# Optimization experiments

Measured on AMD Instinct MI355X. Metric: run time of the kernel, lower is better.

The kernel has to match this reference:

```python
import jax, jax.numpy as jnp
import numpy as np

B, N = 64, 4096

def setup_inputs() -> dict:
    key = jax.random.key(0)
    k1, k2, k3, k4, k5, k6 = jax.random.split(key, 6)
    return {
        "V_mag": jax.random.uniform(k1, (B, N), dtype=jnp.float32, minval=0.9, maxval=1.1),
        "V_ang": 0.3 * jax.random.normal(k2, (B, N), dtype=jnp.float32),
        "P_in": jax.random.normal(k3, (B, N), dtype=jnp.float32),
        "Q_in": jax.random.normal(k4, (B, N), dtype=jnp.float32),
        "G_bus": jax.random.normal(k5, (N, N), dtype=jnp.float32) / np.sqrt(N),
        "B_bus": jax.random.normal(k6, (N, N), dtype=jnp.float32) / np.sqrt(N),
    }

def reference(V_mag, V_ang, P_in, Q_in, G_bus, B_bus):
    # P_i = V_i sum_j V_j (G_ij cos(ti-tj) + B_ij sin(ti-tj))
    # Q_i = V_i sum_j V_j (G_ij sin(ti-tj) - B_ij cos(ti-tj))
    # Angle-addition rewrite (exact): with c_j = V_j cos(t_j), s_j = V_j sin(t_j):
    #   sum_j G_ij V_j cos(ti-tj) = cos(ti)*(G c)_i + sin(ti)*(G s)_i, etc.
    cos_t = jnp.cos(V_ang)  # [B, N]
    sin_t = jnp.sin(V_ang)
    c = V_mag * cos_t       # V_j cos(t_j)
    s = V_mag * sin_t       # V_j sin(t_j)
    Gc = jnp.einsum('ij,bj->bi', G_bus, c)
    Gs = jnp.einsum('ij,bj->bi', G_bus, s)
    Bc = jnp.einsum('ij,bj->bi', B_bus, c)
    Bs = jnp.einsum('ij,bj->bi', B_bus, s)
    # sum_j V_j (G cos + B sin) = cos_ti*(Gc+Bs) + sin_ti*(Gs-Bc)
    P_calc = V_mag * (cos_t * (Gc + Bs) + sin_t * (Gs - Bc))
    # sum_j V_j (G sin - B cos) = sin_ti*(Gc+Bs) - cos_ti*(Gs-Bc)
    Q_calc = V_mag * (sin_t * (Gc + Bs) - cos_t * (Gs - Bc))
    res_P = P_calc - P_in
    res_Q = Q_calc - Q_in
    return (res_P, res_Q)
```

## Files before the change

kernel.cpp:

```cpp
#include <hip/hip_runtime.h>
#include <stdint.h>

#define N_DIM 4096
#define B_DIM 64

typedef __bf16 bf16x8 __attribute__((ext_vector_type(8)));
typedef float floatx4 __attribute__((ext_vector_type(4)));

union FragU { uint4 u; bf16x8 h; };

__device__ __forceinline__ unsigned short f2bf_rne(float f) {
    unsigned int u = __float_as_uint(f);
    u += 0x7fffu + ((u >> 16) & 1u);
    return (unsigned short)(u >> 16);
}

__global__ __launch_bounds__(256) void pf_prep(
        const float* __restrict__ Vmag, const float* __restrict__ Vang,
        unsigned short* __restrict__ c_pk, unsigned short* __restrict__ s_pk,
        float* __restrict__ c_f, float* __restrict__ s_f) {
    int idx = blockIdx.x * 256 + threadIdx.x;
    int b = idx >> 12;
    int j = idx & 4095;
    float sv, cv;
    sincosf(Vang[idx], &sv, &cv);
    float v = Vmag[idx];
    float c = v * cv;
    float s = v * sv;
    c_f[idx] = c;
    s_f[idx] = s;
    int p = (((j >> 3) << 6) + b) * 8 + (j & 7);
    c_pk[p] = f2bf_rne(c);
    s_pk[p] = f2bf_rne(s);
}

__global__ __launch_bounds__(1024, 4) void pf_gemm(
        const float* __restrict__ G, const float* __restrict__ Bm,
        const unsigned short* __restrict__ c_pk, const unsigned short* __restrict__ s_pk,
        const float* __restrict__ c_f, const float* __restrict__ s_f,
        const float* __restrict__ P_in, const float* __restrict__ Q_in,
        float* __restrict__ out) {
    __shared__ float red[2][8][16][66];
    const int tid = threadIdx.x;
    const int wave = tid >> 6;
    const int lane = tid & 63;
    const int n = lane & 15;
    const int quad = lane >> 4;
    const int i0 = blockIdx.x << 4;
    const int kw = wave << 8;

    const float* gp = G  + (size_t)(i0 + n) * N_DIM + kw + (quad << 3);
    const float* bp = Bm + (size_t)(i0 + n) * N_DIM + kw + (quad << 3);
    const unsigned short* cp = c_pk + ((size_t)(((kw >> 3) + quad) << 6) + n) * 8;
    const unsigned short* sp = s_pk + ((size_t)(((kw >> 3) + quad) << 6) + n) * 8;

    floatx4 accX[4], accY[4];
    #pragma unroll
    for (int t = 0; t < 4; ++t) {
        accX[t] = (floatx4){0.f, 0.f, 0.f, 0.f};
        accY[t] = (floatx4){0.f, 0.f, 0.f, 0.f};
    }

    float4 g0 = *(const float4*)gp;
    float4 g1 = *(const float4*)(gp + 4);
    float4 h0 = *(const float4*)bp;
    float4 h1 = *(const float4*)(bp + 4);
    gp += 32; bp += 32;

    #pragma unroll 1
    for (int it = 0; it < 8; ++it) {
        float4 ng0, ng1, nh0, nh1;
        if (it < 7) {
            ng0 = *(const float4*)gp;
            ng1 = *(const float4*)(gp + 4);
            nh0 = *(const float4*)bp;
            nh1 = *(const float4*)(bp + 4);
            gp += 32; bp += 32;
        }

        uint4 cu[4];
        #pragma unroll
        for (int t = 0; t < 4; ++t) cu[t] = *(const uint4*)(cp + t * 128);
        cp += 2048;

        bf16x8 ag, ah;
        ag[0] = (__bf16)g0.x; ag[1] = (__bf16)g0.y; ag[2] = (__bf16)g0.z; ag[3] = (__bf16)g0.w;
        ag[4] = (__bf16)g1.x; ag[5] = (__bf16)g1.y; ag[6] = (__bf16)g1.z; ag[7] = (__bf16)g1.w;
        ah[0] = (__bf16)h0.x; ah[1] = (__bf16)h0.y; ah[2] = (__bf16)h0.z; ah[3] = (__bf16)h0.w;
        ah[4] = (__bf16)h1.x; ah[5] = (__bf16)h1.y; ah[6] = (__bf16)h1.z; ah[7] = (__bf16)h1.w;

        #pragma unroll
        for (int t = 0; t < 4; ++t) {
            FragU cf, nf;
            cf.u = cu[t];
            nf.u.x = cu[t].x ^ 0x80008000u;
            nf.u.y = cu[t].y ^ 0x80008000u;
            nf.u.z = cu[t].z ^ 0x80008000u;
            nf.u.w = cu[t].w ^ 0x80008000u;
            accX[t] = __builtin_amdgcn_mfma_f32_16x16x32_bf16(ag, cf.h, accX[t], 0, 0, 0);
            accY[t] = __builtin_amdgcn_mfma_f32_16x16x32_bf16(ah, nf.h, accY[t], 0, 0, 0);
        }

        uint4 su[4];
        #pragma unroll
        for (int t = 0; t < 4; ++t) su[t] = *(const uint4*)(sp + t * 128);
        sp += 2048;

        #pragma unroll
        for (int t = 0; t < 4; ++t) {
            FragU sf;
            sf.u = su[t];
            accX[t] = __builtin_amdgcn_mfma_f32_16x16x32_bf16(ah, sf.h, accX[t], 0, 0, 0);
            accY[t] = __builtin_amdgcn_mfma_f32_16x16x32_bf16(ag, sf.h, accY[t], 0, 0, 0);
        }

        if (it < 7) { g0 = ng0; g1 = ng1; h0 = nh0; h1 = nh1; }
    }

    if (wave >= 8) {
        #pragma unroll
        for (int t = 0; t < 4; ++t) {
            #pragma unroll
            for (int r = 0; r < 4; ++r) {
                red[0][wave - 8][(quad << 2) + r][(t << 4) + n] = accX[t][r];
                red[1][wave - 8][(quad << 2) + r][(t << 4) + n] = accY[t][r];
            }
        }
    }
    __syncthreads();
    if (wave < 8) {
        #pragma unroll
        for (int t = 0; t < 4; ++t) {
            #pragma unroll
            for (int r = 0; r < 4; ++r) {
                red[0][wave][(quad << 2) + r][(t << 4) + n] += accX[t][r];
                red[1][wave][(quad << 2) + r][(t << 4) + n] += accY[t][r];
            }
        }
    }
    __syncthreads();

    {
        int bb = tid >> 4;
        int m = tid & 15;
        float X = 0.f, Y = 0.f;
        #pragma unroll
        for (int w = 0; w < 8; ++w) {
            X += red[0][w][m][bb];
            Y += red[1][w][m][bb];
        }
        size_t off = (size_t)bb * N_DIM + i0 + m;
        float c = c_f[off], s = s_f[off];
        out[off] = c * X + s * Y - P_in[off];
        out[(size_t)B_DIM * N_DIM + off] = s * X - c * Y - Q_in[off];
    }
}

extern "C" void kernel_launch(void* const* d_in, const int* in_sizes, int n_in,
                              void* d_out, int out_size, void* d_ws, size_t ws_size,
                              hipStream_t stream) {
    const float* Vmag = (const float*)d_in[0];
    const float* Vang = (const float*)d_in[1];
    const float* P_in = (const float*)d_in[2];
    const float* Q_in = (const float*)d_in[3];
    const float* G    = (const float*)d_in[4];
    const float* Bm   = (const float*)d_in[5];
    float* out = (float*)d_out;

    char* ws = (char*)d_ws;
    unsigned short* c_pk = (unsigned short*)(ws);
    unsigned short* s_pk = (unsigned short*)(ws + (512u << 10));
    float* c_f = (float*)(ws + (1u << 20));
    float* s_f = (float*)(ws + (2u << 20));

    hipLaunchKernelGGL(pf_prep, dim3((B_DIM * N_DIM) / 256), dim3(256), 0, stream,
                       Vmag, Vang, c_pk, s_pk, c_f, s_f);
    hipLaunchKernelGGL(pf_gemm, dim3(N_DIM / 16), dim3(1024), 0, stream,
                       G, Bm, c_pk, s_pk, c_f, s_f, P_in, Q_in, out);
}
```

Measured before the change: 171.9 us.

## Stage G/B tiles through LDS via direct global-to-LDS loads with double buffering

The G and B row tiles are now loaded into shared memory with direct global-to-LDS transfers, where each wave fetches a full contiguous row segment, and the loads are double-buffered across eight K chunks. Before, each wave read its own strided K-slice into registers. Waves now read their MFMA A-fragments from LDS, and the K split is interleaved per chunk instead of giving each wave a contiguous 256-column block. The goal is more coalesced HBM traffic and fewer VGPRs spent on prefetch. In exchange it adds a block-wide barrier per chunk and about 132 KB of LDS per block, which likely limits each CU to one resident block.

```diff
diff --git a/kernel.cpp b/kernel.cpp
--- a/kernel.cpp
+++ b/kernel.cpp
@@ -8,6 +8,14 @@
 typedef float floatx4 __attribute__((ext_vector_type(4)));
 
 union FragU { uint4 u; bf16x8 h; };
+
+#define AS1 __attribute__((address_space(1)))
+#define AS3 __attribute__((address_space(3)))
+
+__device__ __forceinline__ void gll16(const float* gp, float* lp) {
+    __builtin_amdgcn_global_load_lds((const AS1 void*)(const void*)gp,
+                                     (AS3 void*)(void*)lp, 16, 0, 0);
+}
 
 __device__ __forceinline__ unsigned short f2bf_rne(float f) {
     unsigned int u = __float_as_uint(f);
@@ -34,25 +42,31 @@
     s_pk[p] = f2bf_rne(s);
 }
 
+#define ROWF 516
+#define MATF (16 * ROWF)
+#define BUFF (2 * MATF)
 __global__ __launch_bounds__(1024, 4) void pf_gemm(
         const float* __restrict__ G, const float* __restrict__ Bm,
         const unsigned short* __restrict__ c_pk, const unsigned short* __restrict__ s_pk,
         const float* __restrict__ c_f, const float* __restrict__ s_f,
         const float* __restrict__ P_in, const float* __restrict__ Q_in,
         float* __restrict__ out) {
-    __shared__ float red[2][8][16][66];
+    __shared__ __align__(16) float lds_f[2 * BUFF];
     const int tid = threadIdx.x;
     const int wave = tid >> 6;
     const int lane = tid & 63;
     const int n = lane & 15;
     const int quad = lane >> 4;
     const int i0 = blockIdx.x << 4;
-    const int kw = wave << 8;
 
-    const float* gp = G  + (size_t)(i0 + n) * N_DIM + kw + (quad << 3);
-    const float* bp = Bm + (size_t)(i0 + n) * N_DIM + kw + (quad << 3);
-    const unsigned short* cp = c_pk + ((size_t)(((kw >> 3) + quad) << 6) + n) * 8;
-    const unsigned short* sp = s_pk + ((size_t)(((kw >> 3) + quad) << 6) + n) * 8;
+    const float* gsrc = G  + (size_t)(i0 + wave) * N_DIM + lane * 4;
+    const float* bsrc = Bm + (size_t)(i0 + wave) * N_DIM + lane * 4;
+    const int stg = wave * ROWF;
+
+    const int aoff = n * ROWF + wave * 32 + quad * 8;
+
+    const unsigned short* cp = c_pk + ((size_t)(((wave << 2) + quad) << 6) + n) * 8;
+    const unsigned short* sp = s_pk + ((size_t)(((wave << 2) + quad) << 6) + n) * 8;
 
     floatx4 accX[4], accY[4];
     #pragma unroll
@@ -61,34 +75,41 @@
         accY[t] = (floatx4){0.f, 0.f, 0.f, 0.f};
     }
 
-    float4 g0 = *(const float4*)gp;
-    float4 g1 = *(const float4*)(gp + 4);
-    float4 h0 = *(const float4*)bp;
-    float4 h1 = *(const float4*)(bp + 4);
-    gp += 32; bp += 32;
+    gll16(gsrc,       lds_f + stg);
+    gll16(gsrc + 256, lds_f + stg + 256);
+    gll16(bsrc,       lds_f + MATF + stg);
+    gll16(bsrc + 256, lds_f + MATF + stg + 256);
 
-    #pragma unroll 1
-    for (int it = 0; it < 8; ++it) {
-        float4 ng0, ng1, nh0, nh1;
-        if (it < 7) {
-            ng0 = *(const float4*)gp;
-            ng1 = *(const float4*)(gp + 4);
-            nh0 = *(const float4*)bp;
-            nh1 = *(const float4*)(bp + 4);
-            gp += 32; bp += 32;
+    #pragma unroll 2
+    for (int c = 0; c < 8; ++c) {
+        const int buf = (c & 1) * BUFF;
+        __syncthreads();
+
+        if (c < 7) {
+            const int nb = ((c + 1) & 1) * BUFF;
+            const float* gs = gsrc + (c + 1) * 512;
+            const float* bs = bsrc + (c + 1) * 512;
+            gll16(gs,       lds_f + nb + stg);
+            gll16(gs + 256, lds_f + nb + stg + 256);
+            gll16(bs,       lds_f + nb + MATF + stg);
+            gll16(bs + 256, lds_f + nb + MATF + stg + 256);
         }
 
-        uint4 cu[4];
-        #pragma unroll
-        for (int t = 0; t < 4; ++t) cu[t] = *(const uint4*)(cp + t * 128);
-        cp += 2048;
-
+        const float* ga = lds_f + buf + aoff;
+        const float* ba = lds_f + buf + MATF + aoff;
+        float4 g0 = *(const float4*)ga;
+        float4 g1 = *(const float4*)(ga + 4);
+        float4 h0 = *(const float4*)ba;
+        float4 h1 = *(const float4*)(ba + 4);
         bf16x8 ag, ah;
         ag[0] = (__bf16)g0.x; ag[1] = (__bf16)g0.y; ag[2] = (__bf16)g0.z; ag[3] = (__bf16)g0.w;
         ag[4] = (__bf16)g1.x; ag[5] = (__bf16)g1.y; ag[6] = (__bf16)g1.z; ag[7] = (__bf16)g1.w;
         ah[0] = (__bf16)h0.x; ah[1] = (__bf16)h0.y; ah[2] = (__bf16)h0.z; ah[3] = (__bf16)h0.w;
         ah[4] = (__bf16)h1.x; ah[5] = (__bf16)h1.y; ah[6] = (__bf16)h1.z; ah[7] = (__bf16)h1.w;
 
+        uint4 cu[4];
+        #pragma unroll
+        for (int t = 0; t < 4; ++t) cu[t] = *(const uint4*)(cp + (size_t)c * 32768 + t * 128);
         #pragma unroll
         for (int t = 0; t < 4; ++t) {
             FragU cf, nf;
@@ -103,9 +124,7 @@
 
         uint4 su[4];
         #pragma unroll
-        for (int t = 0; t < 4; ++t) su[t] = *(const uint4*)(sp + t * 128);
-        sp += 2048;
-
+        for (int t = 0; t < 4; ++t) su[t] = *(const uint4*)(sp + (size_t)c * 32768 + t * 128);
         #pragma unroll
         for (int t = 0; t < 4; ++t) {
             FragU sf;
@@ -113,30 +132,29 @@
             accX[t] = __builtin_amdgcn_mfma_f32_16x16x32_bf16(ah, sf.h, accX[t], 0, 0, 0);
             accY[t] = __builtin_amdgcn_mfma_f32_16x16x32_bf16(ag, sf.h, accY[t], 0, 0, 0);
         }
-
-        if (it < 7) { g0 = ng0; g1 = ng1; h0 = nh0; h1 = nh1; }
     }
 
+    float* red = lds_f;
+    #define RED(x, wp, m, b) red[(((x) * 8 + (wp)) * 16 + (m)) * 66 + (b)]
+    __syncthreads();
     if (wave >= 8) {
         #pragma unroll
-        for (int t = 0; t < 4; ++t) {
+        for (int t = 0; t < 4; ++t)
             #pragma unroll
             for (int r = 0; r < 4; ++r) {
-                red[0][wave - 8][(quad << 2) + r][(t << 4) + n] = accX[t][r];
-                red[1][wave - 8][(quad << 2) + r][(t << 4) + n] = accY[t][r];
+                RED(0, wave - 8, (quad << 2) + r, (t << 4) + n) = accX[t][r];
+                RED(1, wave - 8, (quad << 2) + r, (t << 4) + n) = accY[t][r];
             }
-        }
     }
     __syncthreads();
     if (wave < 8) {
         #pragma unroll
-        for (int t = 0; t < 4; ++t) {
+        for (int t = 0; t < 4; ++t)
             #pragma unroll
             for (int r = 0; r < 4; ++r) {
-                red[0][wave][(quad << 2) + r][(t << 4) + n] += accX[t][r];
-                red[1][wave][(quad << 2) + r][(t << 4) + n] += accY[t][r];
+                RED(0, wave, (quad << 2) + r, (t << 4) + n) += accX[t][r];
+                RED(1, wave, (quad << 2) + r, (t << 4) + n) += accY[t][r];
             }
-        }
     }
     __syncthreads();
 
@@ -146,8 +164,8 @@
         float X = 0.f, Y = 0.f;
         #pragma unroll
         for (int w = 0; w < 8; ++w) {
-            X += red[0][w][m][bb];
-            Y += red[1][w][m][bb];
+            X += RED(0, w, m, bb);
+            Y += RED(1, w, m, bb);
         }
         size_t off = (size_t)bb * N_DIM + i0 + m;
         float c = c_f[off], s = s_f[off];
```

Result: faster. 163.7 us (-4.7%).

## Split GEMM over K across blocks with workspace partials and separate reduce kernel

Applied to the files above, without the earlier changes.

Each block now covers 64 output rows and a quarter of K. Its 16 waves form 4 row stripes by 4 K sub-chunks, so the c/s fragment loads are shared across stripes within the block. Partial X/Y sums go to a workspace and a new pf_reduce kernel sums the four K chunks and applies the cos/sin epilogue. The c/s loads are also hoisted to the top of each loop iteration. The cost is an extra kernel launch plus about 8 MB of workspace traffic.

```diff
diff --git a/kernel.cpp b/kernel.cpp
--- a/kernel.cpp
+++ b/kernel.cpp
@@ -3,6 +3,7 @@
 
 #define N_DIM 4096
 #define B_DIM 64
+#define OUTSZ (B_DIM * N_DIM)
 
 typedef __bf16 bf16x8 __attribute__((ext_vector_type(8)));
 typedef float floatx4 __attribute__((ext_vector_type(4)));
@@ -37,22 +38,26 @@
 __global__ __launch_bounds__(1024, 4) void pf_gemm(
         const float* __restrict__ G, const float* __restrict__ Bm,
         const unsigned short* __restrict__ c_pk, const unsigned short* __restrict__ s_pk,
-        const float* __restrict__ c_f, const float* __restrict__ s_f,
-        const float* __restrict__ P_in, const float* __restrict__ Q_in,
-        float* __restrict__ out) {
-    __shared__ float red[2][8][16][66];
+        float* __restrict__ ws_part) {
+    __shared__ float redX[3][4][16][66];
+    __shared__ float redY[3][4][16][66];
     const int tid = threadIdx.x;
     const int wave = tid >> 6;
     const int lane = tid & 63;
     const int n = lane & 15;
     const int quad = lane >> 4;
-    const int i0 = blockIdx.x << 4;
-    const int kw = wave << 8;
-
-    const float* gp = G  + (size_t)(i0 + n) * N_DIM + kw + (quad << 3);
-    const float* bp = Bm + (size_t)(i0 + n) * N_DIM + kw + (quad << 3);
-    const unsigned short* cp = c_pk + ((size_t)(((kw >> 3) + quad) << 6) + n) * 8;
-    const unsigned short* sp = s_pk + ((size_t)(((kw >> 3) + quad) << 6) + n) * 8;
+    const int kc = blockIdx.x & 3;
+    const int rg = blockIdx.x >> 2;
+    const int stripe = wave & 3;
+    const int kq = wave >> 2;
+
+    const int row = (rg << 6) + (stripe << 4) + n;
+    const int kb = (kc << 10) + (kq << 8);
+
+    const float* gp = G  + (size_t)row * N_DIM + kb + (quad << 3);
+    const float* bp = Bm + (size_t)row * N_DIM + kb + (quad << 3);
+    const unsigned short* cp = c_pk + ((size_t)((kb >> 3) + quad) * 64 + n) * 8;
+    const unsigned short* sp = s_pk + ((size_t)((kb >> 3) + quad) * 64 + n) * 8;
 
     floatx4 accX[4], accY[4];
     #pragma unroll
@@ -69,6 +74,13 @@
 
     #pragma unroll 1
     for (int it = 0; it < 8; ++it) {
+        uint4 cu[4], su[4];
+        #pragma unroll
+        for (int t = 0; t < 4; ++t) cu[t] = *(const uint4*)(cp + t * 128);
+        #pragma unroll
+        for (int t = 0; t < 4; ++t) su[t] = *(const uint4*)(sp + t * 128);
+        cp += 2048; sp += 2048;
+
         float4 ng0, ng1, nh0, nh1;
         if (it < 7) {
             ng0 = *(const float4*)gp;
@@ -77,11 +89,6 @@
             nh1 = *(const float4*)(bp + 4);
             gp += 32; bp += 32;
         }
-
-        uint4 cu[4];
-        #pragma unroll
-        for (int t = 0; t < 4; ++t) cu[t] = *(const uint4*)(cp + t * 128);
-        cp += 2048;
 
         bf16x8 ag, ah;
         ag[0] = (__bf16)g0.x; ag[1] = (__bf16)g0.y; ag[2] = (__bf16)g0.z; ag[3] = (__bf16)g0.w;
@@ -100,12 +107,6 @@
             accX[t] = __builtin_amdgcn_mfma_f32_16x16x32_bf16(ag, cf.h, accX[t], 0, 0, 0);
             accY[t] = __builtin_amdgcn_mfma_f32_16x16x32_bf16(ah, nf.h, accY[t], 0, 0, 0);
         }
-
-        uint4 su[4];
-        #pragma unroll
-        for (int t = 0; t < 4; ++t) su[t] = *(const uint4*)(sp + t * 128);
-        sp += 2048;
-
         #pragma unroll
         for (int t = 0; t < 4; ++t) {
             FragU sf;
@@ -117,43 +118,67 @@
         if (it < 7) { g0 = ng0; g1 = ng1; h0 = nh0; h1 = nh1; }
     }
 
-    if (wave >= 8) {
-        #pragma unroll
-        for (int t = 0; t < 4; ++t) {
+    if (kq > 0) {
+        #pragma unroll
+        for (int t = 0; t < 4; ++t)
             #pragma unroll
             for (int r = 0; r < 4; ++r) {
-                red[0][wave - 8][(quad << 2) + r][(t << 4) + n] = accX[t][r];
-                red[1][wave - 8][(quad << 2) + r][(t << 4) + n] = accY[t][r];
+                redX[kq - 1][stripe][(quad << 2) + r][(t << 4) + n] = accX[t][r];
+                redY[kq - 1][stripe][(quad << 2) + r][(t << 4) + n] = accY[t][r];
             }
-        }
     }
     __syncthreads();
-    if (wave < 8) {
-        #pragma unroll
-        for (int t = 0; t < 4; ++t) {
+    if (kq == 0) {
+        #pragma unroll
+        for (int t = 0; t < 4; ++t)
             #pragma unroll
             for (int r = 0; r < 4; ++r) {
-                red[0][wave][(quad << 2) + r][(t << 4) + n] += accX[t][r];
-                red[1][wave][(quad << 2) + r][(t << 4) + n] += accY[t][r];
+                float x = accX[t][r], y = accY[t][r];
+                #pragma unroll
+                for (int w = 0; w < 3; ++w) {
+                    x += redX[w][stripe][(quad << 2) + r][(t << 4) + n];
+                    y += redY[w][stripe][(quad << 2) + r][(t << 4) + n];
+                }
+                accX[t][r] = x; accY[t][r] = y;
             }
-        }
-    }
-    __syncthreads();
-
-    {
-        int bb = tid >> 4;
-        int m = tid & 15;
-        float X = 0.f, Y = 0.f;
-        #pragma unroll
-        for (int w = 0; w < 8; ++w) {
-            X += red[0][w][m][bb];
-            Y += red[1][w][m][bb];
-        }
-        size_t off = (size_t)bb * N_DIM + i0 + m;
-        float c = c_f[off], s = s_f[off];
-        out[off] = c * X + s * Y - P_in[off];
-        out[(size_t)B_DIM * N_DIM + off] = s * X - c * Y - Q_in[off];
-    }
+        float* wsX = ws_part + (size_t)kc * OUTSZ;
+        float* wsY = ws_part + (size_t)(4 + kc) * OUTSZ;
+        const int rowbase = (rg << 6) + (stripe << 4) + (quad << 2);
+        #pragma unroll
+        for (int t = 0; t < 4; ++t) {
+            size_t off = (size_t)((t << 4) + n) * N_DIM + rowbase;
+            *(float4*)(wsX + off) = (float4){accX[t][0], accX[t][1], accX[t][2], accX[t][3]};
+            *(float4*)(wsY + off) = (float4){accY[t][0], accY[t][1], accY[t][2], accY[t][3]};
+        }
+    }
+}
+
+__global__ __launch_bounds__(256) void pf_reduce(
+        const float* __restrict__ ws_part,
+        const float* __restrict__ c_f, const float* __restrict__ s_f,
+        const float* __restrict__ P_in, const float* __restrict__ Q_in,
+        float* __restrict__ out) {
+    int e = (blockIdx.x * 256 + threadIdx.x) * 4;
+    float4 X = *(const float4*)(ws_part + e);
+    float4 Y = *(const float4*)(ws_part + 4 * OUTSZ + e);
+    #pragma unroll
+    for (int kc = 1; kc < 4; ++kc) {
+        float4 x = *(const float4*)(ws_part + (size_t)kc * OUTSZ + e);
+        float4 y = *(const float4*)(ws_part + (size_t)(4 + kc) * OUTSZ + e);
+        X.x += x.x; X.y += x.y; X.z += x.z; X.w += x.w;
+        Y.x += y.x; Y.y += y.y; Y.z += y.z; Y.w += y.w;
+    }
+    float4 c = *(const float4*)(c_f + e);
+    float4 s = *(const float4*)(s_f + e);
+    float4 P = *(const float4*)(P_in + e);
+    float4 Q = *(const float4*)(Q_in + e);
+    float4 rp, rq;
+    rp.x = c.x * X.x + s.x * Y.x - P.x;  rq.x = s.x * X.x - c.x * Y.x - Q.x;
+    rp.y = c.y * X.y + s.y * Y.y - P.y;  rq.y = s.y * X.y - c.y * Y.y - Q.y;
+    rp.z = c.z * X.z + s.z * Y.z - P.z;  rq.z = s.z * X.z - c.z * Y.z - Q.z;
+    rp.w = c.w * X.w + s.w * Y.w - P.w;  rq.w = s.w * X.w - c.w * Y.w - Q.w;
+    *(float4*)(out + e) = rp;
+    *(float4*)(out + OUTSZ + e) = rq;
 }
 
 extern "C" void kernel_launch(void* const* d_in, const int* in_sizes, int n_in,
@@ -172,9 +197,12 @@
     unsigned short* s_pk = (unsigned short*)(ws + (512u << 10));
     float* c_f = (float*)(ws + (1u << 20));
     float* s_f = (float*)(ws + (2u << 20));
+    float* ws_part = (float*)(ws + (3u << 20));
 
     hipLaunchKernelGGL(pf_prep, dim3((B_DIM * N_DIM) / 256), dim3(256), 0, stream,
                        Vmag, Vang, c_pk, s_pk, c_f, s_f);
-    hipLaunchKernelGGL(pf_gemm, dim3(N_DIM / 16), dim3(1024), 0, stream,
-                       G, Bm, c_pk, s_pk, c_f, s_f, P_in, Q_in, out);
-}
+    hipLaunchKernelGGL(pf_gemm, dim3(256), dim3(1024), 0, stream,
+                       G, Bm, c_pk, s_pk, ws_part);
+    hipLaunchKernelGGL(pf_reduce, dim3(OUTSZ / 1024), dim3(256), 0, stream,
+                       ws_part, c_f, s_f, P_in, Q_in, out);
+}
```

Result: slower. 182.1 us (+6.0%).

## Stage strided G/B row tiles in LDS as bf16 and split epilogue into separate kernel

Applied to the files above, without the earlier changes.

Each block now handles rows i = b + 256*m, loading them with fully coalesced float4 reads across a full 4096-wide row. The rows are converted to bf16 and staged in LDS. G and B are processed in two sequential passes, with the LDS tile reused, instead of being interleaved per wave. Raw X/Y sums go to a workspace, and a new vectorized elementwise kernel applies the cos/sin combination and subtracts P_in/Q_in. This aims to improve global read coalescing for G and B, at the cost of an extra kernel launch, a workspace round-trip, and about 131KB of LDS per block, which limits occupancy to one block per CU.

```diff
diff --git a/kernel.cpp b/kernel.cpp
--- a/kernel.cpp
+++ b/kernel.cpp
@@ -3,6 +3,7 @@
 
 #define N_DIM 4096
 #define B_DIM 64
+#define OUTSZ (B_DIM * N_DIM)
 
 typedef __bf16 bf16x8 __attribute__((ext_vector_type(8)));
 typedef float floatx4 __attribute__((ext_vector_type(4)));
@@ -34,126 +35,137 @@
     s_pk[p] = f2bf_rne(s);
 }
 
+#define ROWH 4104
 __global__ __launch_bounds__(1024, 4) void pf_gemm(
         const float* __restrict__ G, const float* __restrict__ Bm,
         const unsigned short* __restrict__ c_pk, const unsigned short* __restrict__ s_pk,
-        const float* __restrict__ c_f, const float* __restrict__ s_f,
-        const float* __restrict__ P_in, const float* __restrict__ Q_in,
-        float* __restrict__ out) {
-    __shared__ float red[2][8][16][66];
+        float* __restrict__ wsX, float* __restrict__ wsY) {
+    __shared__ __align__(16) unsigned short lds_a[16 * ROWH];
     const int tid = threadIdx.x;
     const int wave = tid >> 6;
     const int lane = tid & 63;
     const int n = lane & 15;
     const int quad = lane >> 4;
-    const int i0 = blockIdx.x << 4;
+    const int b = blockIdx.x;
+
+    floatx4 acc1[4], acc2[4];
+    #pragma unroll
+    for (int t = 0; t < 4; ++t) {
+        acc1[t] = (floatx4){0.f, 0.f, 0.f, 0.f};
+        acc2[t] = (floatx4){0.f, 0.f, 0.f, 0.f};
+    }
+
     const int kw = wave << 8;
 
-    const float* gp = G  + (size_t)(i0 + n) * N_DIM + kw + (quad << 3);
-    const float* bp = Bm + (size_t)(i0 + n) * N_DIM + kw + (quad << 3);
-    const unsigned short* cp = c_pk + ((size_t)(((kw >> 3) + quad) << 6) + n) * 8;
-    const unsigned short* sp = s_pk + ((size_t)(((kw >> 3) + quad) << 6) + n) * 8;
+    #pragma unroll 1
+    for (int pass = 0; pass < 2; ++pass) {
+        const float* M = (pass == 0) ? G : Bm;
+        const float* base = M + (size_t)b * N_DIM + (tid << 2);
+        #pragma unroll 4
+        for (int s = 0; s < 16; ++s) {
+            float4 v = *(const float4*)(base + ((size_t)s << 20));
+            unsigned short w0 = f2bf_rne(v.x), w1 = f2bf_rne(v.y);
+            unsigned short w2 = f2bf_rne(v.z), w3 = f2bf_rne(v.w);
+            ushort4 pk = {w0, w1, w2, w3};
+            *(ushort4*)&lds_a[s * ROWH + (tid << 2)] = pk;
+        }
+        __syncthreads();
 
-    floatx4 accX[4], accY[4];
-    #pragma unroll
-    for (int t = 0; t < 4; ++t) {
-        accX[t] = (floatx4){0.f, 0.f, 0.f, 0.f};
-        accY[t] = (floatx4){0.f, 0.f, 0.f, 0.f};
+        #pragma unroll 1
+        for (int st = 0; st < 8; ++st) {
+            const int k0 = kw + (st << 5);
+            bf16x8 am = *(const bf16x8*)&lds_a[(size_t)n * ROWH + k0 + (quad << 3)];
+            const int kg = (k0 >> 3) + quad;
+            const unsigned short* cpp = c_pk + ((size_t)kg << 9) + (n << 3);
+            const unsigned short* spp = s_pk + ((size_t)kg << 9) + (n << 3);
+            uint4 cu[4], su[4];
+            #pragma unroll
+            for (int t = 0; t < 4; ++t) cu[t] = *(const uint4*)(cpp + (t << 7));
+            #pragma unroll
+            for (int t = 0; t < 4; ++t) su[t] = *(const uint4*)(spp + (t << 7));
+
+            if (pass == 0) {
+                #pragma unroll
+                for (int t = 0; t < 4; ++t) {
+                    FragU cf, sf;
+                    cf.u = cu[t]; sf.u = su[t];
+                    acc1[t] = __builtin_amdgcn_mfma_f32_16x16x32_bf16(am, cf.h, acc1[t], 0, 0, 0);
+                    acc2[t] = __builtin_amdgcn_mfma_f32_16x16x32_bf16(am, sf.h, acc2[t], 0, 0, 0);
+                }
+            } else {
+                #pragma unroll
+                for (int t = 0; t < 4; ++t) {
+                    FragU sf, nf;
+                    sf.u = su[t];
+                    nf.u.x = cu[t].x ^ 0x80008000u;
+                    nf.u.y = cu[t].y ^ 0x80008000u;
+                    nf.u.z = cu[t].z ^ 0x80008000u;
+                    nf.u.w = cu[t].w ^ 0x80008000u;
+                    acc1[t] = __builtin_amdgcn_mfma_f32_16x16x32_bf16(am, sf.h, acc1[t], 0, 0, 0);
+                    acc2[t] = __builtin_amdgcn_mfma_f32_16x16x32_bf16(am, nf.h, acc2[t], 0, 0, 0);
+                }
+            }
+        }
+        __syncthreads();
     }
 
-    float4 g0 = *(const float4*)gp;
-    float4 g1 = *(const float4*)(gp + 4);
-    float4 h0 = *(const float4*)bp;
-    float4 h1 = *(const float4*)(bp + 4);
-    gp += 32; bp += 32;
-
-    #pragma unroll 1
-    for (int it = 0; it < 8; ++it) {
-        float4 ng0, ng1, nh0, nh1;
-        if (it < 7) {
-            ng0 = *(const float4*)gp;
-            ng1 = *(const float4*)(gp + 4);
-            nh0 = *(const float4*)bp;
-            nh1 = *(const float4*)(bp + 4);
-            gp += 32; bp += 32;
-        }
-
-        uint4 cu[4];
-        #pragma unroll
-        for (int t = 0; t < 4; ++t) cu[t] = *(const uint4*)(cp + t * 128);
-        cp += 2048;
-
-        bf16x8 ag, ah;
-        ag[0] = (__bf16)g0.x; ag[1] = (__bf16)g0.y; ag[2] = (__bf16)g0.z; ag[3] = (__bf16)g0.w;
-        ag[4] = (__bf16)g1.x; ag[5] = (__bf16)g1.y; ag[6] = (__bf16)g1.z; ag[7] = (__bf16)g1.w;
-        ah[0] = (__bf16)h0.x; ah[1] = (__bf16)h0.y; ah[2] = (__bf16)h0.z; ah[3] = (__bf16)h0.w;
-        ah[4] = (__bf16)h1.x; ah[5] = (__bf16)h1.y; ah[6] = (__bf16)h1.z; ah[7] = (__bf16)h1.w;
-
-        #pragma unroll
-        for (int t = 0; t < 4; ++t) {
-            FragU cf, nf;
-            cf.u = cu[t];
-            nf.u.x = cu[t].x ^ 0x80008000u;
-            nf.u.y = cu[t].y ^ 0x80008000u;
-            nf.u.z = cu[t].z ^ 0x80008000u;
-            nf.u.w = cu[t].w ^ 0x80008000u;
-            accX[t] = __builtin_amdgcn_mfma_f32_16x16x32_bf16(ag, cf.h, accX[t], 0, 0, 0);
-            accY[t] = __builtin_amdgcn_mfma_f32_16x16x32_bf16(ah, nf.h, accY[t], 0, 0, 0);
-        }
-
-        uint4 su[4];
-        #pragma unroll
-        for (int t = 0; t < 4; ++t) su[t] = *(const uint4*)(sp + t * 128);
-        sp += 2048;
-
-        #pragma unroll
-        for (int t = 0; t < 4; ++t) {
-            FragU sf;
-            sf.u = su[t];
-            accX[t] = __builtin_amdgcn_mfma_f32_16x16x32_bf16(ah, sf.h, accX[t], 0, 0, 0);
-            accY[t] = __builtin_amdgcn_mfma_f32_16x16x32_bf16(ag, sf.h, accY[t], 0, 0, 0);
-        }
-
-        if (it < 7) { g0 = ng0; g1 = ng1; h0 = nh0; h1 = nh1; }
-    }
-
+    float* red = (float*)lds_a;
+    #define RD(x, w_, m, bb) red[((((x) * 8 + (w_)) * 16 + (m)) * 66) + (bb)]
     if (wave >= 8) {
         #pragma unroll
-        for (int t = 0; t < 4; ++t) {
+        for (int t = 0; t < 4; ++t)
             #pragma unroll
             for (int r = 0; r < 4; ++r) {
-                red[0][wave - 8][(quad << 2) + r][(t << 4) + n] = accX[t][r];
-                red[1][wave - 8][(quad << 2) + r][(t << 4) + n] = accY[t][r];
+                RD(0, wave - 8, (quad << 2) + r, (t << 4) + n) = acc1[t][r];
+                RD(1, wave - 8, (quad << 2) + r, (t << 4) + n) = acc2[t][r];
             }
-        }
     }
     __syncthreads();
     if (wave < 8) {
         #pragma unroll
-        for (int t = 0; t < 4; ++t) {
+        for (int t = 0; t < 4; ++t)
             #pragma unroll
             for (int r = 0; r < 4; ++r) {
-                red[0][wave][(quad << 2) + r][(t << 4) + n] += accX[t][r];
-                red[1][wave][(quad << 2) + r][(t << 4) + n] += accY[t][r];
+                RD(0, wave, (quad << 2) + r, (t << 4) + n) += acc1[t][r];
+                RD(1, wave, (quad << 2) + r, (t << 4) + n) += acc2[t][r];
             }
-        }
     }
     __syncthreads();
 
     {
-        int bb = tid >> 4;
-        int m = tid & 15;
+        const int bb = tid >> 4;
+        const int m = tid & 15;
         float X = 0.f, Y = 0.f;
         #pragma unroll
         for (int w = 0; w < 8; ++w) {
-            X += red[0][w][m][bb];
-            Y += red[1][w][m][bb];
+            X += RD(0, w, m, bb);
+            Y += RD(1, w, m, bb);
         }
-        size_t off = (size_t)bb * N_DIM + i0 + m;
-        float c = c_f[off], s = s_f[off];
-        out[off] = c * X + s * Y - P_in[off];
-        out[(size_t)B_DIM * N_DIM + off] = s * X - c * Y - Q_in[off];
+        size_t off = (size_t)bb * N_DIM + b + (m << 8);
+        wsX[off] = X;
+        wsY[off] = Y;
     }
+}
+
+__global__ __launch_bounds__(256) void pf_reduce(
+        const float* __restrict__ wsX, const float* __restrict__ wsY,
+        const float* __restrict__ c_f, const float* __restrict__ s_f,
+        const float* __restrict__ P_in, const float* __restrict__ Q_in,
+        float* __restrict__ out) {
+    int e = (blockIdx.x * 256 + threadIdx.x) * 4;
+    float4 X = *(const float4*)(wsX + e);
+    float4 Y = *(const float4*)(wsY + e);
+    float4 c = *(const float4*)(c_f + e);
+    float4 s = *(const float4*)(s_f + e);
+    float4 P = *(const float4*)(P_in + e);
+    float4 Q = *(const float4*)(Q_in + e);
+    float4 rp, rq;
+    rp.x = c.x * X.x + s.x * Y.x - P.x;  rq.x = s.x * X.x - c.x * Y.x - Q.x;
+    rp.y = c.y * X.y + s.y * Y.y - P.y;  rq.y = s.y * X.y - c.y * Y.y - Q.y;
+    rp.z = c.z * X.z + s.z * Y.z - P.z;  rq.z = s.z * X.z - c.z * Y.z - Q.z;
+    rp.w = c.w * X.w + s.w * Y.w - P.w;  rq.w = s.w * X.w - c.w * Y.w - Q.w;
+    *(float4*)(out + e) = rp;
+    *(float4*)(out + OUTSZ + e) = rq;
 }
 
 extern "C" void kernel_launch(void* const* d_in, const int* in_sizes, int n_in,
@@ -172,9 +184,13 @@
     unsigned short* s_pk = (unsigned short*)(ws + (512u << 10));
     float* c_f = (float*)(ws + (1u << 20));
     float* s_f = (float*)(ws + (2u << 20));
+    float* wsX = (float*)(ws + (3u << 20));
+    float* wsY = (float*)(ws + (4u << 20));
 
     hipLaunchKernelGGL(pf_prep, dim3((B_DIM * N_DIM) / 256), dim3(256), 0, stream,
                        Vmag, Vang, c_pk, s_pk, c_f, s_f);
-    hipLaunchKernelGGL(pf_gemm, dim3(N_DIM / 16), dim3(1024), 0, stream,
-                       G, Bm, c_pk, s_pk, c_f, s_f, P_in, Q_in, out);
+    hipLaunchKernelGGL(pf_gemm, dim3(256), dim3(1024), 0, stream,
+                       G, Bm, c_pk, s_pk, wsX, wsY);
+    hipLaunchKernelGGL(pf_reduce, dim3(OUTSZ / 1024), dim3(256), 0, stream,
+                       wsX, wsY, c_f, s_f, P_in, Q_in, out);
 }
```

Measured after the change: 184.5 us. +7.4%, slower.
